# Kernel optimization log

Hardware: AMD Instinct MI355X
Metric: run time of the kernel (lower is better)

## Reference

```python
import jax, jax.numpy as jnp
import numpy as np

B, N, DIM = 32, 1025, 768
H, D = 12, 64
THETA = 100.0


def setup_inputs() -> dict:
    key = jax.random.key(0)
    k0, k1, k2, k3 = jax.random.split(key, 4)
    x = jax.random.normal(k0, (B, N, DIM), dtype=jnp.float32)
    W_qkv = jax.random.normal(k1, (3 * H * D, DIM), dtype=jnp.float32) * 0.02
    W_out = jax.random.normal(k2, (DIM, H * D), dtype=jnp.float32) * 0.02
    b_out = jnp.zeros((DIM,), dtype=jnp.float32)
    # performer random projection buffer: randn(num_features, dim_head) * sqrt(2/dim_head)
    projection = jax.random.normal(k3, (D, D), dtype=jnp.float32) * np.sqrt(2.0 / D)
    # RoPE frequencies for content tokens (n-1 positions, dim_head/2 pairs)
    inv_freq = 1.0 / (THETA ** (np.arange(0, D, 2, dtype=np.float32) / D))  # (D/2,)
    t = np.arange(N - 1, dtype=np.float32)
    angles = np.outer(t, inv_freq)  # (N-1, D/2)
    freqs_cos = jnp.asarray(np.cos(angles), dtype=jnp.float32)
    freqs_sin = jnp.asarray(np.sin(angles), dtype=jnp.float32)
    return {"x": x, "W_qkv": W_qkv, "W_out": W_out, "b_out": b_out,
            "projection": projection, "freqs_cos": freqs_cos, "freqs_sin": freqs_sin}


def reference(x, W_qkv, W_out, b_out, projection, freqs_cos, freqs_sin):
    b, n, _ = x.shape
    h, d = H, D
    # qkv projection and split: 'b n (qkv h d) -> qkv b h n d'
    qkv = jnp.einsum('bnf,gf->bng', x, W_qkv).reshape(b, n, 3, h, d)
    q = jnp.transpose(qkv[:, :, 0], (0, 2, 1, 3))  # (b,h,n,d)
    k = jnp.transpose(qkv[:, :, 1], (0, 2, 1, 3))
    v = jnp.transpose(qkv[:, :, 2], (0, 2, 1, 3))

    def rope(t):
        # rotate content tokens (skip CLS token 0); complex mult as real math
        tc = t[:, :, 1:].reshape(b, h, n - 1, d // 2, 2)
        ev, od = tc[..., 0], tc[..., 1]
        c = freqs_cos[None, None]
        s = freqs_sin[None, None]
        rot = jnp.stack([ev * c - od * s, ev * s + od * c], axis=-1).reshape(b, h, n - 1, d)
        return jnp.concatenate([t[:, :, :1], rot], axis=2)

    q = rope(q)
    k = rope(k)

    def feature_map(t):
        # x * d^{-1/4}, project with (feat, d), relu + eps
        tp = jnp.einsum('bhnd,jd->bhnj', t * (d ** -0.25), projection)
        return jax.nn.relu(tp) + 1e-6

    qf = feature_map(q)
    kf = feature_map(k)

    # non-causal linear attention
    k_sum = kf.sum(axis=-2)                              # (b,h,j)
    context = jnp.einsum('bhnd,bhne->bhde', kf, v)       # (b,h,feat,d)
    D_inv = 1.0 / jnp.einsum('bhnd,bhd->bhn', qf, k_sum)
    out = jnp.einsum('bhde,bhnd,bhn->bhne', context, qf, D_inv)  # (b,h,n,d)

    out = jnp.transpose(out, (0, 2, 1, 3)).reshape(b, n, h * d)
    return jnp.einsum('bnf,gf->bng', out, W_out) + b_out
```

## Files before the change

kernel.cpp:

```cpp
#include <hip/hip_runtime.h>
#include <stdint.h>
#include <stddef.h>

typedef __bf16 bft;
typedef __bf16 bf16x4 __attribute__((ext_vector_type(4)));
typedef __bf16 bf16x8 __attribute__((ext_vector_type(8)));
typedef float f32x4 __attribute__((ext_vector_type(4)));

#define NH 12
#define HD 64
#define SEQ 1025
#define NB 32
#define DMODEL 768
#define MROWS (NB * SEQ)
#define BHN (NB * NH)
#define BSTR 1040
#define MP (NB * BSTR)
#define SEQP 1056

__device__ __forceinline__ void gl_lds16(const void* g, void* l) {
  __builtin_amdgcn_global_load_lds(
      (const __attribute__((address_space(1))) void*)g,
      (__attribute__((address_space(3))) void*)l, 16, 0, 0);
}

__device__ __forceinline__ bf16x4 ds_tr16(const bft* p, int boff) {
  bf16x4 d;
  asm volatile("ds_read_b64_tr_b16 %0, %1 offset:%2"
               : "=v"(d)
               : "v"((const __attribute__((address_space(3))) bft*)p), "i"(boff)
               : "memory");
  return d;
}

__device__ __forceinline__ void lgkm0() {
  asm volatile("s_waitcnt lgkmcnt(0)" ::: "memory");
}

__global__ __launch_bounds__(256) void k_cast(
    const float* __restrict__ S, bft* __restrict__ D, int n4) {
  int i = blockIdx.x * 256 + threadIdx.x;
  if (i < n4) {
    f32x4 v = *(const f32x4*)(S + (size_t)i * 4);
    bf16x4 o;
    o[0] = (bft)v[0]; o[1] = (bft)v[1]; o[2] = (bft)v[2]; o[3] = (bft)v[3];
    *(bf16x4*)(D + (size_t)i * 4) = o;
  }
}

__global__ __launch_bounds__(256) void k_padzero(bft* __restrict__ KFT, bft* __restrict__ VT) {
  int r = blockIdx.x * 256 + threadIdx.x;
  if (r < BHN * 64) {
    bft* a = KFT + (size_t)r * SEQP + 1025;
    bft* b = VT + (size_t)r * SEQP + 1025;
#pragma unroll
    for (int i = 0; i < 31; ++i) { a[i] = (bft)0.f; b[i] = (bft)0.f; }
  }
}

__global__ __launch_bounds__(256) void k_ropeprep(
    const float* __restrict__ FC, const float* __restrict__ FS,
    float* __restrict__ FCP, float* __restrict__ FSP) {
  int i = blockIdx.x * 256 + threadIdx.x;
  if (i < 1040 * 32) {
    int n = i >> 5;
    int fj = i & 31;
    float c = 1.f, s = 0.f;
    if (n >= 1 && n <= 1024) {
      c = FC[(n - 1) * 32 + fj];
      s = FS[(n - 1) * 32 + fj];
    }
    FCP[i] = c;
    FSP[i] = s;
  }
}

__global__ __launch_bounds__(256) void k_qkv_gemm(
    const bft* __restrict__ X, const bft* __restrict__ W,
    const bft* __restrict__ P,
    const float* __restrict__ FCP, const float* __restrict__ FSP,
    bft* __restrict__ QF, bft* __restrict__ KFT, bft* __restrict__ VT) {
  __shared__ __align__(16) bft sA[128 * 64];
  __shared__ __align__(16) bft sB[128 * 64];
  __shared__ __align__(16) bft sP[64 * 64];
  const int tid = threadIdx.x;
  const int lane = tid & 63;
  const int lm = lane & 15;
  const int quad = lane >> 4;
  const int wid = tid >> 6;
  const int wm = (wid & 1) << 6;
  const int wn = (wid >> 1) << 6;
  const int lin = blockIdx.x;
  const int logical = (lin & 7) * 585 + (lin >> 3);
  const int cb = logical % 18;
  const int rb = logical / 18;
  const int m0 = rb * 128;
  const int n0 = cb * 128;
  const int sw = lm & 7;
  const int o0 = (quad ^ sw) << 3;
  const int o1 = ((4 + quad) ^ sw) << 3;

#pragma unroll
  for (int it = 0; it < 2; it++) {
    int c = it * 256 + tid;
    int row = c >> 3;
    int col = ((c & 7) ^ (row & 7)) << 3;
    gl_lds16(P + row * 64 + col, sP + c * 8);
  }

  const bft* aptr[4];
  const bft* bptr[4];
#pragma unroll
  for (int it = 0; it < 4; it++) {
    int c = it * 256 + tid;
    int row = c >> 3;
    int col = ((c & 7) ^ (row & 7)) << 3;
    int ar = m0 + row;
    int b2 = ar / BSTR;
    int nn = ar - b2 * BSTR;
    if (nn > 1024) nn = 1024;
    aptr[it] = X + (size_t)(b2 * SEQ + nn) * DMODEL + col;
    bptr[it] = W + (size_t)(n0 + row) * DMODEL + col;
  }

  f32x4 acc[4][4] = {};

  for (int kt = 0; kt < DMODEL; kt += 64) {
#pragma unroll
    for (int it = 0; it < 4; it++) {
      int c = it * 256 + tid;
      gl_lds16(aptr[it], sA + c * 8);
      gl_lds16(bptr[it], sB + c * 8);
      aptr[it] += 64;
      bptr[it] += 64;
    }
    __syncthreads();
#pragma unroll
    for (int kk = 0; kk < 2; kk++) {
      const int off = kk ? o1 : o0;
      bf16x8 af[4], bb[4];
#pragma unroll
      for (int i = 0; i < 4; i++)
        af[i] = *(const bf16x8*)(sA + (wm + i * 16 + lm) * 64 + off);
#pragma unroll
      for (int j = 0; j < 4; j++)
        bb[j] = *(const bf16x8*)(sB + (wn + j * 16 + lm) * 64 + off);
#pragma unroll
      for (int i = 0; i < 4; i++)
#pragma unroll
        for (int j = 0; j < 4; j++)
          acc[i][j] = __builtin_amdgcn_mfma_f32_16x16x32_bf16(af[i], bb[j], acc[i][j], 0, 0, 0);
    }
    __syncthreads();
  }

  const int s = cb / 6;
  const int h = ((n0 + wn) - s * DMODEL) >> 6;

  bft* tt = sA + wid * 1024;
  const bft* tl = tt + quad * 128 + lm * 4;

  if (s < 2) {
    const float sgn = (lm & 1) ? 1.f : -1.f;
#pragma unroll
    for (int i = 0; i < 4; i++) {
      const int tbase = m0 + wm + i * 16;
      const int bb2 = tbase / BSTR;
      const int nb = tbase - bb2 * BSTR;
#pragma unroll
      for (int j = 0; j < 4; j++) {
        const int fj = (j * 16 + lm) >> 1;
        const int d = j * 16 + lm;
        bf16x4 w;
#pragma unroll
        for (int r = 0; r < 4; r++) {
          float v = acc[i][j][r];
          float pv = __shfl_xor(v, 1);
          int n = nb + quad * 4 + r;
          float cc = FCP[n * 32 + fj];
          float ss = FSP[n * 32 + fj];
          w[r] = (bft)fmaf(pv, sgn * ss, v * cc);
        }
        *(bf16x4*)(tt + d * 16 + quad * 4) = w;
      }
      lgkm0();
      bf16x4 i0a = ds_tr16(tl, 0);
      bf16x4 i0b = ds_tr16(tl, 128);
      bf16x4 i1a = ds_tr16(tl, 1024);
      bf16x4 i1b = ds_tr16(tl, 1152);
      lgkm0();
      __builtin_amdgcn_sched_barrier(0);
      bf16x8 af0, af1;
#pragma unroll
      for (int e = 0; e < 4; e++) {
        af0[e] = i0a[e]; af0[e + 4] = i0b[e];
        af1[e] = i1a[e]; af1[e + 4] = i1b[e];
      }

      if (s == 0) {
        const int n = nb + lm;
        const bool valid = (n < SEQ);
        bft* dst = QF + ((size_t)(bb2 * NH + h) * SEQ + n) * HD;
#pragma unroll
        for (int j2 = 0; j2 < 4; j2++) {
          bf16x8 p0 = *(const bf16x8*)(sP + (j2 * 16 + lm) * 64 + o0);
          bf16x8 p1 = *(const bf16x8*)(sP + (j2 * 16 + lm) * 64 + o1);
          f32x4 fa = {0.f, 0.f, 0.f, 0.f};
          fa = __builtin_amdgcn_mfma_f32_16x16x32_bf16(p0, af0, fa, 0, 0, 0);
          fa = __builtin_amdgcn_mfma_f32_16x16x32_bf16(p1, af1, fa, 0, 0, 0);
          bf16x4 o;
#pragma unroll
          for (int r = 0; r < 4; r++) {
            float v = fa[r] * 0.35355339f;
            o[r] = (bft)(fmaxf(v, 0.f) + 1e-6f);
          }
          if (valid) *(bf16x4*)(dst + j2 * 16 + quad * 4) = o;
        }
      } else {
        const int nq = nb + quad * 4;
#pragma unroll
        for (int j2 = 0; j2 < 4; j2++) {
          bf16x8 p0 = *(const bf16x8*)(sP + (j2 * 16 + lm) * 64 + o0);
          bf16x8 p1 = *(const bf16x8*)(sP + (j2 * 16 + lm) * 64 + o1);
          f32x4 fa = {0.f, 0.f, 0.f, 0.f};
          fa = __builtin_amdgcn_mfma_f32_16x16x32_bf16(af0, p0, fa, 0, 0, 0);
          fa = __builtin_amdgcn_mfma_f32_16x16x32_bf16(af1, p1, fa, 0, 0, 0);
          bf16x4 o;
#pragma unroll
          for (int r = 0; r < 4; r++) {
            float v = fa[r] * 0.35355339f;
            o[r] = (bft)(fmaxf(v, 0.f) + 1e-6f);
          }
          bft* rowp = KFT + ((size_t)(bb2 * NH + h) * 64 + j2 * 16 + lm) * SEQP;
          if (nq + 3 <= 1024) {
            *(bf16x4*)(rowp + nq) = o;
          } else {
#pragma unroll
            for (int r = 0; r < 4; r++)
              if (nq + r <= 1024) rowp[nq + r] = o[r];
          }
        }
      }
    }
  } else {
#pragma unroll
    for (int i = 0; i < 4; i++) {
      const int tbase = m0 + wm + i * 16;
      const int bb2 = tbase / BSTR;
      const int nb = tbase - bb2 * BSTR;
      const int nq = nb + quad * 4;
#pragma unroll
      for (int j = 0; j < 4; j++) {
        bf16x4 o;
#pragma unroll
        for (int r = 0; r < 4; r++) o[r] = (bft)acc[i][j][r];
        bft* rowp = VT + ((size_t)(bb2 * NH + h) * 64 + j * 16 + lm) * SEQP;
        if (nq + 3 <= 1024) {
          *(bf16x4*)(rowp + nq) = o;
        } else {
#pragma unroll
          for (int r = 0; r < 4; r++)
            if (nq + r <= 1024) rowp[nq + r] = o[r];
        }
      }
    }
  }
}

__global__ __launch_bounds__(256) void k_context(
    const bft* __restrict__ KFT, const bft* __restrict__ VT,
    float* __restrict__ CTX, float* __restrict__ KSUM) {
  __shared__ __align__(16) bft sK[64 * 32];
  __shared__ __align__(16) bft sV[64 * 32];
  const int tid = threadIdx.x;
  const int lane = tid & 63;
  const int lm = lane & 15;
  const int quad = lane >> 4;
  const int wid = tid >> 6;
  const int bh = blockIdx.x;
  const int y = blockIdx.y;
  const int c0 = (33 * y) / 4;
  const int c1 = (33 * (y + 1)) / 4;
  const bft* kb = KFT + (size_t)bh * 64 * SEQP;
  const bft* vb = VT + (size_t)bh * 64 * SEQP;
  const int f0 = wid * 16;
  const int srow = tid >> 2;
  const int sch = (tid & 3) * 8;

  bf16x8 ones;
#pragma unroll
  for (int e = 0; e < 8; e++) ones[e] = (bft)1.0f;

  f32x4 acc[4] = {};
  f32x4 ak = {0.f, 0.f, 0.f, 0.f};

  for (int c = c0; c < c1; ++c) {
    const int t0 = c * 32;
    gl_lds16(kb + (size_t)srow * SEQP + t0 + sch, sK + tid * 8);
    gl_lds16(vb + (size_t)srow * SEQP + t0 + sch, sV + tid * 8);
    __syncthreads();
    bf16x8 a = *(const bf16x8*)(sK + (f0 + lm) * 32 + quad * 8);
    ak = __builtin_amdgcn_mfma_f32_16x16x32_bf16(a, ones, ak, 0, 0, 0);
#pragma unroll
    for (int j = 0; j < 4; j++) {
      bf16x8 b = *(const bf16x8*)(sV + (j * 16 + lm) * 32 + quad * 8);
      acc[j] = __builtin_amdgcn_mfma_f32_16x16x32_bf16(a, b, acc[j], 0, 0, 0);
    }
    __syncthreads();
  }

  float* cp = CTX + (size_t)bh * 4096;
#pragma unroll
  for (int j = 0; j < 4; j++)
#pragma unroll
    for (int r = 0; r < 4; r++)
      atomicAdd(&cp[(f0 + quad * 4 + r) * 64 + j * 16 + lm], acc[j][r]);
  if (lm == 0) {
#pragma unroll
    for (int r = 0; r < 4; r++)
      atomicAdd(&KSUM[bh * 64 + f0 + quad * 4 + r], ak[r]);
  }
}

__global__ __launch_bounds__(256) void k_ctxprep(
    const float* __restrict__ CTX, const float* __restrict__ KSUM,
    bft* __restrict__ CTH, bft* __restrict__ CTL,
    bft* __restrict__ KTH, bft* __restrict__ KTL) {
  const int bh = blockIdx.x;
  const int tid = threadIdx.x;
  const int e = tid >> 2;
  const int g = tid & 3;
  const float* src = CTX + (size_t)bh * 4096 + e;
  bf16x8 h0, l0, h1, l1;
#pragma unroll
  for (int k = 0; k < 16; ++k) {
    float v = src[(g * 16 + k) * 64];
    bft hi = (bft)v;
    bft lo = (bft)(v - (float)hi);
    if (k < 8) { h0[k] = hi; l0[k] = lo; }
    else       { h1[k - 8] = hi; l1[k - 8] = lo; }
  }
  const int c0 = (2 * g) ^ (e & 7);
  const int c1 = (2 * g + 1) ^ (e & 7);
  bft* dh = CTH + (size_t)bh * 4096 + e * 64;
  bft* dl = CTL + (size_t)bh * 4096 + e * 64;
  *(bf16x8*)(dh + c0 * 8) = h0;
  *(bf16x8*)(dh + c1 * 8) = h1;
  *(bf16x8*)(dl + c0 * 8) = l0;
  *(bf16x8*)(dl + c1 * 8) = l1;
  if (tid < 64) {
    float v = KSUM[bh * 64 + tid];
    bft hi = (bft)v;
    KTH[bh * 64 + tid] = hi;
    KTL[bh * 64 + tid] = (bft)(v - (float)hi);
  }
}

__global__ __launch_bounds__(256) void k_qside(
    const bft* __restrict__ QF, const bft* __restrict__ CTH,
    const bft* __restrict__ CTL, const bft* __restrict__ KTH,
    const bft* __restrict__ KTL, bft* __restrict__ ATTN) {
  __shared__ __align__(16) bft sq[128 * 64];
  __shared__ __align__(16) bft sh[64 * 64];
  __shared__ __align__(16) bft sl[64 * 64];
  const int tid = threadIdx.x;
  const int lane = tid & 63;
  const int lm = lane & 15;
  const int quad = lane >> 4;
  const int wid = tid >> 6;
  const int bh = blockIdx.x;
  const int n0 = blockIdx.y * 128;
  const bft* qf = QF + ((size_t)bh * SEQ + n0) * HD;

#pragma unroll
  for (int it = 0; it < 4; it++) {
    int c = it * 256 + tid;
    int row = c >> 3;
    int col = ((c & 7) ^ (row & 7)) << 3;
    gl_lds16(qf + (size_t)row * 64 + col, sq + c * 8);
  }
#pragma unroll
  for (int it = 0; it < 2; it++) {
    int c = it * 256 + tid;
    gl_lds16(CTH + (size_t)bh * 4096 + c * 8, sh + c * 8);
    gl_lds16(CTL + (size_t)bh * 4096 + c * 8, sl + c * 8);
  }
  bf16x8 kh0 = *(const bf16x8*)(KTH + bh * 64 + quad * 8);
  bf16x8 kh1 = *(const bf16x8*)(KTH + bh * 64 + 32 + quad * 8);
  bf16x8 kl0 = *(const bf16x8*)(KTL + bh * 64 + quad * 8);
  bf16x8 kl1 = *(const bf16x8*)(KTL + bh * 64 + 32 + quad * 8);
  bf16x8 zz = {};
  bf16x8 ad0 = (lm == 0) ? kh0 : (lm == 1) ? kl0 : zz;
  bf16x8 ad1 = (lm == 0) ? kh1 : (lm == 1) ? kl1 : zz;
  __syncthreads();

  bf16x8 ah[4][2], al[4][2];
#pragma unroll
  for (int eb = 0; eb < 4; eb++)
#pragma unroll
    for (int kc = 0; kc < 2; kc++) {
      const int off = ((quad + 4 * kc) ^ (lm & 7)) * 8;
      ah[eb][kc] = *(const bf16x8*)(sh + (eb * 16 + lm) * 64 + off);
      al[eb][kc] = *(const bf16x8*)(sl + (eb * 16 + lm) * 64 + off);
    }

  const int b = bh / NH;
  const int h = bh - b * NH;
#pragma unroll
  for (int tb2 = 0; tb2 < 2; tb2++) {
    const int tok0 = (wid * 2 + tb2) * 16;
    const int roff = (tok0 + lm) * 64;
    bf16x8 bq0 = *(const bf16x8*)(sq + roff + ((quad) ^ (lm & 7)) * 8);
    bf16x8 bq1 = *(const bf16x8*)(sq + roff + ((4 + quad) ^ (lm & 7)) * 8);
    f32x4 dacc = {0.f, 0.f, 0.f, 0.f};
    dacc = __builtin_amdgcn_mfma_f32_16x16x32_bf16(ad0, bq0, dacc, 0, 0, 0);
    dacc = __builtin_amdgcn_mfma_f32_16x16x32_bf16(ad1, bq1, dacc, 0, 0, 0);
    const float den = __shfl(dacc[0] + dacc[1], lm);
    const float dinv = 1.0f / den;
    f32x4 fa[4] = {};
#pragma unroll
    for (int eb = 0; eb < 4; eb++) {
      fa[eb] = __builtin_amdgcn_mfma_f32_16x16x32_bf16(ah[eb][0], bq0, fa[eb], 0, 0, 0);
      fa[eb] = __builtin_amdgcn_mfma_f32_16x16x32_bf16(al[eb][0], bq0, fa[eb], 0, 0, 0);
      fa[eb] = __builtin_amdgcn_mfma_f32_16x16x32_bf16(ah[eb][1], bq1, fa[eb], 0, 0, 0);
      fa[eb] = __builtin_amdgcn_mfma_f32_16x16x32_bf16(al[eb][1], bq1, fa[eb], 0, 0, 0);
    }
    const int n = n0 + tok0 + lm;
    if (n < SEQ) {
      bft* dst = ATTN + ((size_t)(b * SEQ + n)) * DMODEL + h * 64;
#pragma unroll
      for (int eb = 0; eb < 4; eb++) {
        bf16x4 o;
#pragma unroll
        for (int r = 0; r < 4; r++) o[r] = (bft)(fa[eb][r] * dinv);
        *(bf16x4*)(dst + eb * 16 + quad * 4) = o;
      }
    }
  }
}

__global__ __launch_bounds__(256) void k_out_gemm(
    const bft* __restrict__ A, const bft* __restrict__ W,
    const float* __restrict__ BIAS, float* __restrict__ OUT) {
  __shared__ __align__(16) bft sA[128 * 64];
  __shared__ __align__(16) bft sB[128 * 64];
  const int tid = threadIdx.x;
  const int lane = tid & 63;
  const int lm = lane & 15;
  const int quad = lane >> 4;
  const int wid = tid >> 6;
  const int wm = (wid & 1) << 6;
  const int wn = (wid >> 1) << 6;
  const int lin = blockIdx.x;
  const int xcd = lin & 7;
  const int slot = lin >> 3;
  const int base = (xcd < 6) ? xcd * 193 : 6 * 193 + (xcd - 6) * 192;
  const int logical = base + slot;
  const int cb = logical % 6;
  const int rb = logical / 6;
  const int m0 = rb * 128;
  const int n0 = cb * 128;
  const int sw = lm & 7;
  const int o0 = (quad ^ sw) << 3;
  const int o1 = ((4 + quad) ^ sw) << 3;

  const bft* aptr[4];
  const bft* bptr[4];
#pragma unroll
  for (int it = 0; it < 4; it++) {
    int c = it * 256 + tid;
    int row = c >> 3;
    int col = ((c & 7) ^ (row & 7)) << 3;
    int ar = m0 + row;
    if (ar >= MROWS) ar = MROWS - 1;
    aptr[it] = A + (size_t)ar * DMODEL + col;
    bptr[it] = W + (size_t)(n0 + row) * DMODEL + col;
  }

  f32x4 acc[4][4] = {};

  for (int kt = 0; kt < DMODEL; kt += 64) {
#pragma unroll
    for (int it = 0; it < 4; it++) {
      int c = it * 256 + tid;
      gl_lds16(aptr[it], sA + c * 8);
      gl_lds16(bptr[it], sB + c * 8);
      aptr[it] += 64;
      bptr[it] += 64;
    }
    __syncthreads();
#pragma unroll
    for (int kk = 0; kk < 2; kk++) {
      const int off = kk ? o1 : o0;
      bf16x8 af[4], bb[4];
#pragma unroll
      for (int i = 0; i < 4; i++)
        af[i] = *(const bf16x8*)(sA + (wm + i * 16 + lm) * 64 + off);
#pragma unroll
      for (int j = 0; j < 4; j++)
        bb[j] = *(const bf16x8*)(sB + (wn + j * 16 + lm) * 64 + off);
#pragma unroll
      for (int i = 0; i < 4; i++)
#pragma unroll
        for (int j = 0; j < 4; j++)
          acc[i][j] = __builtin_amdgcn_mfma_f32_16x16x32_bf16(bb[j], af[i], acc[i][j], 0, 0, 0);
    }
    __syncthreads();
  }

#pragma unroll
  for (int i = 0; i < 4; i++) {
    const int m = m0 + wm + i * 16 + lm;
    if (m < MROWS) {
#pragma unroll
      for (int j = 0; j < 4; j++) {
        const int g = n0 + wn + j * 16 + quad * 4;
        f32x4 bias = *(const f32x4*)(BIAS + g);
        f32x4 o;
#pragma unroll
        for (int r = 0; r < 4; r++) o[r] = acc[i][j][r] + bias[r];
        *(f32x4*)(OUT + (size_t)m * DMODEL + g) = o;
      }
    }
  }
}

extern "C" void kernel_launch(void* const* d_in, const int* in_sizes, int n_in,
                              void* d_out, int out_size, void* d_ws, size_t ws_size,
                              hipStream_t stream) {
  const float* x = (const float*)d_in[0];
  const float* wqkv = (const float*)d_in[1];
  const float* wout = (const float*)d_in[2];
  const float* bout = (const float*)d_in[3];
  const float* proj = (const float*)d_in[4];
  const float* fc = (const float*)d_in[5];
  const float* fs = (const float*)d_in[6];
  float* outp = (float*)d_out;

  char* ws = (char*)d_ws;
  const size_t xb_bytes = (size_t)MROWS * DMODEL * 2;
  const size_t qf_bytes = (size_t)BHN * SEQ * HD * 2;
  const size_t kt_bytes = (size_t)BHN * 64 * SEQP * 2;
  const size_t wqkvb_bytes = (size_t)3 * DMODEL * DMODEL * 2;
  const size_t woutb_bytes = (size_t)DMODEL * DMODEL * 2;
  const size_t projb_bytes = 8192;
  const size_t ctx_bytes = (size_t)BHN * 64 * 64 * 4;
  const size_t ks_bytes = (size_t)BHN * 64 * 4;
  const size_t ctt_bytes = (size_t)BHN * 64 * 64 * 2;
  const size_t kst_bytes = (size_t)BHN * 64 * 2;
  const size_t ftab_bytes = (size_t)1040 * 32 * 4;

  bft* xb = (bft*)ws;
  bft* qfb = (bft*)(ws + xb_bytes);
  bft* kft = (bft*)(ws + xb_bytes + qf_bytes);
  bft* vt = (bft*)(ws + xb_bytes + qf_bytes + kt_bytes);
  bft* wqkvb = (bft*)(ws + xb_bytes + qf_bytes + 2 * kt_bytes);
  bft* woutb = (bft*)(ws + xb_bytes + qf_bytes + 2 * kt_bytes + wqkvb_bytes);
  bft* projb = (bft*)(ws + xb_bytes + qf_bytes + 2 * kt_bytes + wqkvb_bytes + woutb_bytes);
  float* fcp = (float*)(ws + xb_bytes + qf_bytes + 2 * kt_bytes + wqkvb_bytes + woutb_bytes + projb_bytes);
  float* fsp = (float*)(ws + xb_bytes + qf_bytes + 2 * kt_bytes + wqkvb_bytes + woutb_bytes + projb_bytes + ftab_bytes);

  float* ctx = (float*)ws;
  float* ksum = (float*)(ws + ctx_bytes);
  bft* cth = (bft*)(ws + ctx_bytes + ks_bytes);
  bft* ctl = (bft*)(ws + ctx_bytes + ks_bytes + ctt_bytes);
  bft* kth = (bft*)(ws + ctx_bytes + ks_bytes + 2 * ctt_bytes);
  bft* ktl = (bft*)(ws + ctx_bytes + ks_bytes + 2 * ctt_bytes + kst_bytes);
  bft* attn = kft;

  dim3 blk(256);
  k_cast<<<dim3((MROWS * DMODEL / 4 + 255) / 256), blk, 0, stream>>>(x, xb, MROWS * DMODEL / 4);
  k_cast<<<dim3((3 * DMODEL * DMODEL / 4 + 255) / 256), blk, 0, stream>>>(wqkv, wqkvb, 3 * DMODEL * DMODEL / 4);
  k_cast<<<dim3((DMODEL * DMODEL / 4 + 255) / 256), blk, 0, stream>>>(wout, woutb, DMODEL * DMODEL / 4);
  k_cast<<<dim3((HD * HD / 4 + 255) / 256), blk, 0, stream>>>(proj, projb, HD * HD / 4);
  k_padzero<<<dim3((BHN * 64 + 255) / 256), blk, 0, stream>>>(kft, vt);
  k_ropeprep<<<dim3(130), blk, 0, stream>>>(fc, fs, fcp, fsp);

  k_qkv_gemm<<<dim3(4680), blk, 0, stream>>>(xb, wqkvb, projb, fcp, fsp, qfb, kft, vt);

  hipMemsetAsync(ctx, 0, ctx_bytes + ks_bytes, stream);

  k_context<<<dim3(BHN, 4), blk, 0, stream>>>(kft, vt, ctx, ksum);
  k_ctxprep<<<dim3(BHN), blk, 0, stream>>>(ctx, ksum, cth, ctl, kth, ktl);
  k_qside<<<dim3(BHN, 9), blk, 0, stream>>>(qfb, cth, ctl, kth, ktl, attn);
  k_out_gemm<<<dim3(1542), blk, 0, stream>>>(attn, woutb, bout, outp);
  (void)in_sizes; (void)n_in; (void)out_size; (void)ws_size;
}
```

Baseline: 515.9 us.

## Fuse prep kernels, drop atomics and LDS staging in context and q-side kernels

```diff
diff --git a/kernel.cpp b/kernel.cpp
--- a/kernel.cpp
+++ b/kernel.cpp
@@ -37,41 +37,57 @@
   asm volatile("s_waitcnt lgkmcnt(0)" ::: "memory");
 }
 
-__global__ __launch_bounds__(256) void k_cast(
-    const float* __restrict__ S, bft* __restrict__ D, int n4) {
-  int i = blockIdx.x * 256 + threadIdx.x;
-  if (i < n4) {
-    f32x4 v = *(const f32x4*)(S + (size_t)i * 4);
-    bf16x4 o;
-    o[0] = (bft)v[0]; o[1] = (bft)v[1]; o[2] = (bft)v[2]; o[3] = (bft)v[3];
-    *(bf16x4*)(D + (size_t)i * 4) = o;
-  }
-}
-
-__global__ __launch_bounds__(256) void k_padzero(bft* __restrict__ KFT, bft* __restrict__ VT) {
-  int r = blockIdx.x * 256 + threadIdx.x;
-  if (r < BHN * 64) {
+#define S0P 6297600
+#define S1P (S0P + 442368)
+#define S2P (S1P + 147456)
+#define S3P (S2P + 1024)
+#define S4P (S3P + 24576)
+#define S5P (S4P + 33280)
+
+__global__ __launch_bounds__(256) void k_prep(
+    const float* __restrict__ X, const float* __restrict__ WQKV,
+    const float* __restrict__ WOUT, const float* __restrict__ PROJ,
+    const float* __restrict__ FC, const float* __restrict__ FS,
+    bft* __restrict__ XB, bft* __restrict__ WQKVB, bft* __restrict__ WOUTB,
+    bft* __restrict__ PROJB, bft* __restrict__ KFT, bft* __restrict__ VT,
+    float* __restrict__ FCP, float* __restrict__ FSP) {
+  const int i = blockIdx.x * 256 + threadIdx.x;
+  if (i < S0P) {
+    f32x4 v = *(const f32x4*)(X + (size_t)i * 4);
+    bf16x4 o; o[0]=(bft)v[0]; o[1]=(bft)v[1]; o[2]=(bft)v[2]; o[3]=(bft)v[3];
+    *(bf16x4*)(XB + (size_t)i * 4) = o;
+  } else if (i < S1P) {
+    int k = i - S0P;
+    f32x4 v = *(const f32x4*)(WQKV + (size_t)k * 4);
+    bf16x4 o; o[0]=(bft)v[0]; o[1]=(bft)v[1]; o[2]=(bft)v[2]; o[3]=(bft)v[3];
+    *(bf16x4*)(WQKVB + (size_t)k * 4) = o;
+  } else if (i < S2P) {
+    int k = i - S1P;
+    f32x4 v = *(const f32x4*)(WOUT + (size_t)k * 4);
+    bf16x4 o; o[0]=(bft)v[0]; o[1]=(bft)v[1]; o[2]=(bft)v[2]; o[3]=(bft)v[3];
+    *(bf16x4*)(WOUTB + (size_t)k * 4) = o;
+  } else if (i < S3P) {
+    int k = i - S2P;
+    f32x4 v = *(const f32x4*)(PROJ + (size_t)k * 4);
+    bf16x4 o; o[0]=(bft)v[0]; o[1]=(bft)v[1]; o[2]=(bft)v[2]; o[3]=(bft)v[3];
+    *(bf16x4*)(PROJB + (size_t)k * 4) = o;
+  } else if (i < S4P) {
+    int r = i - S3P;
     bft* a = KFT + (size_t)r * SEQP + 1025;
     bft* b = VT + (size_t)r * SEQP + 1025;
 #pragma unroll
-    for (int i = 0; i < 31; ++i) { a[i] = (bft)0.f; b[i] = (bft)0.f; }
-  }
-}
-
-__global__ __launch_bounds__(256) void k_ropeprep(
-    const float* __restrict__ FC, const float* __restrict__ FS,
-    float* __restrict__ FCP, float* __restrict__ FSP) {
-  int i = blockIdx.x * 256 + threadIdx.x;
-  if (i < 1040 * 32) {
-    int n = i >> 5;
-    int fj = i & 31;
+    for (int q = 0; q < 31; ++q) { a[q] = (bft)0.f; b[q] = (bft)0.f; }
+  } else if (i < S5P) {
+    int k = i - S4P;
+    int n = k >> 5;
+    int fj = k & 31;
     float c = 1.f, s = 0.f;
     if (n >= 1 && n <= 1024) {
       c = FC[(n - 1) * 32 + fj];
       s = FS[(n - 1) * 32 + fj];
     }
-    FCP[i] = c;
-    FSP[i] = s;
+    FCP[k] = c;
+    FSP[k] = s;
   }
 }
 
@@ -80,9 +96,9 @@
     const bft* __restrict__ P,
     const float* __restrict__ FCP, const float* __restrict__ FSP,
     bft* __restrict__ QF, bft* __restrict__ KFT, bft* __restrict__ VT) {
-  __shared__ __align__(16) bft sA[128 * 64];
-  __shared__ __align__(16) bft sB[128 * 64];
-  __shared__ __align__(16) bft sP[64 * 64];
+  __shared__ __align__(16) bft sAll[128 * 64 * 2];
+  bft* sA = sAll;
+  bft* sB = sAll + 8192;
   const int tid = threadIdx.x;
   const int lane = tid & 63;
   const int lm = lane & 15;
@@ -100,14 +116,6 @@
   const int o0 = (quad ^ sw) << 3;
   const int o1 = ((4 + quad) ^ sw) << 3;
 
-#pragma unroll
-  for (int it = 0; it < 2; it++) {
-    int c = it * 256 + tid;
-    int row = c >> 3;
-    int col = ((c & 7) ^ (row & 7)) << 3;
-    gl_lds16(P + row * 64 + col, sP + c * 8);
-  }
-
   const bft* aptr[4];
   const bft* bptr[4];
 #pragma unroll
@@ -157,81 +165,94 @@
   const int s = cb / 6;
   const int h = ((n0 + wn) - s * DMODEL) >> 6;
 
-  bft* tt = sA + wid * 1024;
+  bft* tt = sAll + wid * 4096;
   const bft* tl = tt + quad * 128 + lm * 4;
 
   if (s < 2) {
     const float sgn = (lm & 1) ? 1.f : -1.f;
+    int bb2s[4], nbs[4];
 #pragma unroll
     for (int i = 0; i < 4; i++) {
       const int tbase = m0 + wm + i * 16;
-      const int bb2 = tbase / BSTR;
-      const int nb = tbase - bb2 * BSTR;
+      bb2s[i] = tbase / BSTR;
+      nbs[i] = tbase - bb2s[i] * BSTR;
 #pragma unroll
       for (int j = 0; j < 4; j++) {
-        const int fj = (j * 16 + lm) >> 1;
         const int d = j * 16 + lm;
+        const int fj = d >> 1;
         bf16x4 w;
 #pragma unroll
         for (int r = 0; r < 4; r++) {
           float v = acc[i][j][r];
           float pv = __shfl_xor(v, 1);
-          int n = nb + quad * 4 + r;
+          int n = nbs[i] + quad * 4 + r;
           float cc = FCP[n * 32 + fj];
           float ss = FSP[n * 32 + fj];
           w[r] = (bft)fmaf(pv, sgn * ss, v * cc);
         }
-        *(bf16x4*)(tt + d * 16 + quad * 4) = w;
-      }
-      lgkm0();
-      bf16x4 i0a = ds_tr16(tl, 0);
-      bf16x4 i0b = ds_tr16(tl, 128);
-      bf16x4 i1a = ds_tr16(tl, 1024);
-      bf16x4 i1b = ds_tr16(tl, 1152);
-      lgkm0();
-      __builtin_amdgcn_sched_barrier(0);
-      bf16x8 af0, af1;
+        *(bf16x4*)(tt + i * 1024 + d * 16 + quad * 4) = w;
+      }
+    }
+    lgkm0();
+    bf16x4 t0[4], t1[4], t2[4], t3[4];
+#pragma unroll
+    for (int i = 0; i < 4; i++) {
+      t0[i] = ds_tr16(tl, i * 2048 + 0);
+      t1[i] = ds_tr16(tl, i * 2048 + 128);
+      t2[i] = ds_tr16(tl, i * 2048 + 1024);
+      t3[i] = ds_tr16(tl, i * 2048 + 1152);
+    }
+    lgkm0();
+    __builtin_amdgcn_sched_barrier(0);
+    bf16x8 af[4][2];
+#pragma unroll
+    for (int i = 0; i < 4; i++) {
 #pragma unroll
       for (int e = 0; e < 4; e++) {
-        af0[e] = i0a[e]; af0[e + 4] = i0b[e];
-        af1[e] = i1a[e]; af1[e + 4] = i1b[e];
-      }
-
-      if (s == 0) {
-        const int n = nb + lm;
-        const bool valid = (n < SEQ);
-        bft* dst = QF + ((size_t)(bb2 * NH + h) * SEQ + n) * HD;
-#pragma unroll
-        for (int j2 = 0; j2 < 4; j2++) {
-          bf16x8 p0 = *(const bf16x8*)(sP + (j2 * 16 + lm) * 64 + o0);
-          bf16x8 p1 = *(const bf16x8*)(sP + (j2 * 16 + lm) * 64 + o1);
+        af[i][0][e] = t0[i][e]; af[i][0][e + 4] = t1[i][e];
+        af[i][1][e] = t2[i][e]; af[i][1][e + 4] = t3[i][e];
+      }
+    }
+
+    if (s == 0) {
+#pragma unroll
+      for (int j2 = 0; j2 < 4; j2++) {
+        bf16x8 p0 = *(const bf16x8*)(P + (j2 * 16 + lm) * 64 + quad * 8);
+        bf16x8 p1 = *(const bf16x8*)(P + (j2 * 16 + lm) * 64 + 32 + quad * 8);
+#pragma unroll
+        for (int i = 0; i < 4; i++) {
           f32x4 fa = {0.f, 0.f, 0.f, 0.f};
-          fa = __builtin_amdgcn_mfma_f32_16x16x32_bf16(p0, af0, fa, 0, 0, 0);
-          fa = __builtin_amdgcn_mfma_f32_16x16x32_bf16(p1, af1, fa, 0, 0, 0);
+          fa = __builtin_amdgcn_mfma_f32_16x16x32_bf16(p0, af[i][0], fa, 0, 0, 0);
+          fa = __builtin_amdgcn_mfma_f32_16x16x32_bf16(p1, af[i][1], fa, 0, 0, 0);
           bf16x4 o;
 #pragma unroll
           for (int r = 0; r < 4; r++) {
             float v = fa[r] * 0.35355339f;
             o[r] = (bft)(fmaxf(v, 0.f) + 1e-6f);
           }
-          if (valid) *(bf16x4*)(dst + j2 * 16 + quad * 4) = o;
+          const int n = nbs[i] + lm;
+          if (n < SEQ)
+            *(bf16x4*)(QF + ((size_t)(bb2s[i] * NH + h) * SEQ + n) * HD + j2 * 16 + quad * 4) = o;
         }
-      } else {
-        const int nq = nb + quad * 4;
-#pragma unroll
-        for (int j2 = 0; j2 < 4; j2++) {
-          bf16x8 p0 = *(const bf16x8*)(sP + (j2 * 16 + lm) * 64 + o0);
-          bf16x8 p1 = *(const bf16x8*)(sP + (j2 * 16 + lm) * 64 + o1);
+      }
+    } else {
+#pragma unroll
+      for (int j2 = 0; j2 < 4; j2++) {
+        bf16x8 p0 = *(const bf16x8*)(P + (j2 * 16 + lm) * 64 + quad * 8);
+        bf16x8 p1 = *(const bf16x8*)(P + (j2 * 16 + lm) * 64 + 32 + quad * 8);
+#pragma unroll
+        for (int i = 0; i < 4; i++) {
           f32x4 fa = {0.f, 0.f, 0.f, 0.f};
-          fa = __builtin_amdgcn_mfma_f32_16x16x32_bf16(af0, p0, fa, 0, 0, 0);
-          fa = __builtin_amdgcn_mfma_f32_16x16x32_bf16(af1, p1, fa, 0, 0, 0);
+          fa = __builtin_amdgcn_mfma_f32_16x16x32_bf16(af[i][0], p0, fa, 0, 0, 0);
+          fa = __builtin_amdgcn_mfma_f32_16x16x32_bf16(af[i][1], p1, fa, 0, 0, 0);
           bf16x4 o;
 #pragma unroll
           for (int r = 0; r < 4; r++) {
             float v = fa[r] * 0.35355339f;
             o[r] = (bft)(fmaxf(v, 0.f) + 1e-6f);
           }
-          bft* rowp = KFT + ((size_t)(bb2 * NH + h) * 64 + j2 * 16 + lm) * SEQP;
+          const int nq = nbs[i] + quad * 4;
+          bft* rowp = KFT + ((size_t)(bb2s[i] * NH + h) * 64 + j2 * 16 + lm) * SEQP;
           if (nq + 3 <= 1024) {
             *(bf16x4*)(rowp + nq) = o;
           } else {
@@ -269,9 +290,7 @@
 
 __global__ __launch_bounds__(256) void k_context(
     const bft* __restrict__ KFT, const bft* __restrict__ VT,
-    float* __restrict__ CTX, float* __restrict__ KSUM) {
-  __shared__ __align__(16) bft sK[64 * 32];
-  __shared__ __align__(16) bft sV[64 * 32];
+    float* __restrict__ CTXP, float* __restrict__ KSP) {
   const int tid = threadIdx.x;
   const int lane = tid & 63;
   const int lm = lane & 15;
@@ -281,11 +300,9 @@
   const int y = blockIdx.y;
   const int c0 = (33 * y) / 4;
   const int c1 = (33 * (y + 1)) / 4;
-  const bft* kb = KFT + (size_t)bh * 64 * SEQP;
-  const bft* vb = VT + (size_t)bh * 64 * SEQP;
+  const bft* kb = KFT + (size_t)bh * 64 * SEQP + (size_t)(wid * 16 + lm) * SEQP + quad * 8;
+  const bft* vb = VT + (size_t)bh * 64 * SEQP + (size_t)lm * SEQP + quad * 8;
   const int f0 = wid * 16;
-  const int srow = tid >> 2;
-  const int sch = (tid & 3) * 8;
 
   bf16x8 ones;
 #pragma unroll
@@ -294,62 +311,64 @@
   f32x4 acc[4] = {};
   f32x4 ak = {0.f, 0.f, 0.f, 0.f};
 
+#pragma unroll 2
   for (int c = c0; c < c1; ++c) {
     const int t0 = c * 32;
-    gl_lds16(kb + (size_t)srow * SEQP + t0 + sch, sK + tid * 8);
-    gl_lds16(vb + (size_t)srow * SEQP + t0 + sch, sV + tid * 8);
-    __syncthreads();
-    bf16x8 a = *(const bf16x8*)(sK + (f0 + lm) * 32 + quad * 8);
+    bf16x8 a = *(const bf16x8*)(kb + t0);
     ak = __builtin_amdgcn_mfma_f32_16x16x32_bf16(a, ones, ak, 0, 0, 0);
 #pragma unroll
     for (int j = 0; j < 4; j++) {
-      bf16x8 b = *(const bf16x8*)(sV + (j * 16 + lm) * 32 + quad * 8);
+      bf16x8 b = *(const bf16x8*)(vb + (size_t)j * 16 * SEQP + t0);
       acc[j] = __builtin_amdgcn_mfma_f32_16x16x32_bf16(a, b, acc[j], 0, 0, 0);
     }
-    __syncthreads();
-  }
-
-  float* cp = CTX + (size_t)bh * 4096;
+  }
+
+  float* cp = CTXP + ((size_t)(y * BHN) + bh) * 4096;
 #pragma unroll
   for (int j = 0; j < 4; j++)
-#pragma unroll
-    for (int r = 0; r < 4; r++)
-      atomicAdd(&cp[(f0 + quad * 4 + r) * 64 + j * 16 + lm], acc[j][r]);
-  if (lm == 0) {
-#pragma unroll
-    for (int r = 0; r < 4; r++)
-      atomicAdd(&KSUM[bh * 64 + f0 + quad * 4 + r], ak[r]);
-  }
+    *(f32x4*)(cp + (j * 16 + lm) * 64 + f0 + quad * 4) = acc[j];
+  if (lm == 0)
+    *(f32x4*)(KSP + ((size_t)(y * BHN) + bh) * 64 + f0 + quad * 4) = ak;
 }
 
 __global__ __launch_bounds__(256) void k_ctxprep(
-    const float* __restrict__ CTX, const float* __restrict__ KSUM,
+    const float* __restrict__ CTXP, const float* __restrict__ KSP,
     bft* __restrict__ CTH, bft* __restrict__ CTL,
     bft* __restrict__ KTH, bft* __restrict__ KTL) {
   const int bh = blockIdx.x;
   const int tid = threadIdx.x;
   const int e = tid >> 2;
-  const int g = tid & 3;
-  const float* src = CTX + (size_t)bh * 4096 + e;
+  const int fc = tid & 3;
+  f32x4 s[4] = {};
+#pragma unroll
+  for (int y = 0; y < 4; y++) {
+    const float* src = CTXP + ((size_t)(y * BHN) + bh) * 4096 + e * 64 + fc * 16;
+#pragma unroll
+    for (int q = 0; q < 4; q++) {
+      f32x4 v = *(const f32x4*)(src + q * 4);
+      s[q][0] += v[0]; s[q][1] += v[1]; s[q][2] += v[2]; s[q][3] += v[3];
+    }
+  }
   bf16x8 h0, l0, h1, l1;
 #pragma unroll
-  for (int k = 0; k < 16; ++k) {
-    float v = src[(g * 16 + k) * 64];
+  for (int k = 0; k < 8; k++) {
+    float v = s[k >> 2][k & 3];
     bft hi = (bft)v;
-    bft lo = (bft)(v - (float)hi);
-    if (k < 8) { h0[k] = hi; l0[k] = lo; }
-    else       { h1[k - 8] = hi; l1[k - 8] = lo; }
-  }
-  const int c0 = (2 * g) ^ (e & 7);
-  const int c1 = (2 * g + 1) ^ (e & 7);
-  bft* dh = CTH + (size_t)bh * 4096 + e * 64;
-  bft* dl = CTL + (size_t)bh * 4096 + e * 64;
-  *(bf16x8*)(dh + c0 * 8) = h0;
-  *(bf16x8*)(dh + c1 * 8) = h1;
-  *(bf16x8*)(dl + c0 * 8) = l0;
-  *(bf16x8*)(dl + c1 * 8) = l1;
+    h0[k] = hi; l0[k] = (bft)(v - (float)hi);
+    float v2 = s[2 + (k >> 2)][k & 3];
+    bft hi2 = (bft)v2;
+    h1[k] = hi2; l1[k] = (bft)(v2 - (float)hi2);
+  }
+  bft* dh = CTH + (size_t)bh * 4096 + e * 64 + fc * 16;
+  bft* dl = CTL + (size_t)bh * 4096 + e * 64 + fc * 16;
+  *(bf16x8*)(dh) = h0;
+  *(bf16x8*)(dh + 8) = h1;
+  *(bf16x8*)(dl) = l0;
+  *(bf16x8*)(dl + 8) = l1;
   if (tid < 64) {
-    float v = KSUM[bh * 64 + tid];
+    float v = 0.f;
+#pragma unroll
+    for (int y = 0; y < 4; y++) v += KSP[((size_t)(y * BHN) + bh) * 64 + tid];
     bft hi = (bft)v;
     KTH[bh * 64 + tid] = hi;
     KTL[bh * 64 + tid] = (bft)(v - (float)hi);
@@ -360,9 +379,6 @@
     const bft* __restrict__ QF, const bft* __restrict__ CTH,
     const bft* __restrict__ CTL, const bft* __restrict__ KTH,
     const bft* __restrict__ KTL, bft* __restrict__ ATTN) {
-  __shared__ __align__(16) bft sq[128 * 64];
-  __shared__ __align__(16) bft sh[64 * 64];
-  __shared__ __align__(16) bft sl[64 * 64];
   const int tid = threadIdx.x;
   const int lane = tid & 63;
   const int lm = lane & 15;
@@ -372,19 +388,6 @@
   const int n0 = blockIdx.y * 128;
   const bft* qf = QF + ((size_t)bh * SEQ + n0) * HD;
 
-#pragma unroll
-  for (int it = 0; it < 4; it++) {
-    int c = it * 256 + tid;
-    int row = c >> 3;
-    int col = ((c & 7) ^ (row & 7)) << 3;
-    gl_lds16(qf + (size_t)row * 64 + col, sq + c * 8);
-  }
-#pragma unroll
-  for (int it = 0; it < 2; it++) {
-    int c = it * 256 + tid;
-    gl_lds16(CTH + (size_t)bh * 4096 + c * 8, sh + c * 8);
-    gl_lds16(CTL + (size_t)bh * 4096 + c * 8, sl + c * 8);
-  }
   bf16x8 kh0 = *(const bf16x8*)(KTH + bh * 64 + quad * 8);
   bf16x8 kh1 = *(const bf16x8*)(KTH + bh * 64 + 32 + quad * 8);
   bf16x8 kl0 = *(const bf16x8*)(KTL + bh * 64 + quad * 8);
@@ -392,16 +395,15 @@
   bf16x8 zz = {};
   bf16x8 ad0 = (lm == 0) ? kh0 : (lm == 1) ? kl0 : zz;
   bf16x8 ad1 = (lm == 0) ? kh1 : (lm == 1) ? kl1 : zz;
-  __syncthreads();
 
   bf16x8 ah[4][2], al[4][2];
 #pragma unroll
   for (int eb = 0; eb < 4; eb++)
 #pragma unroll
     for (int kc = 0; kc < 2; kc++) {
-      const int off = ((quad + 4 * kc) ^ (lm & 7)) * 8;
-      ah[eb][kc] = *(const bf16x8*)(sh + (eb * 16 + lm) * 64 + off);
-      al[eb][kc] = *(const bf16x8*)(sl + (eb * 16 + lm) * 64 + off);
+      const size_t off = (size_t)bh * 4096 + (eb * 16 + lm) * 64 + kc * 32 + quad * 8;
+      ah[eb][kc] = *(const bf16x8*)(CTH + off);
+      al[eb][kc] = *(const bf16x8*)(CTL + off);
     }
 
   const int b = bh / NH;
@@ -409,9 +411,9 @@
 #pragma unroll
   for (int tb2 = 0; tb2 < 2; tb2++) {
     const int tok0 = (wid * 2 + tb2) * 16;
-    const int roff = (tok0 + lm) * 64;
-    bf16x8 bq0 = *(const bf16x8*)(sq + roff + ((quad) ^ (lm & 7)) * 8);
-    bf16x8 bq1 = *(const bf16x8*)(sq + roff + ((4 + quad) ^ (lm & 7)) * 8);
+    const int rr = (n0 + tok0 + lm <= 1024) ? (tok0 + lm) : (1024 - n0);
+    bf16x8 bq0 = *(const bf16x8*)(qf + (size_t)rr * 64 + quad * 8);
+    bf16x8 bq1 = *(const bf16x8*)(qf + (size_t)rr * 64 + 32 + quad * 8);
     f32x4 dacc = {0.f, 0.f, 0.f, 0.f};
     dacc = __builtin_amdgcn_mfma_f32_16x16x32_bf16(ad0, bq0, dacc, 0, 0, 0);
     dacc = __builtin_amdgcn_mfma_f32_16x16x32_bf16(ad1, bq1, dacc, 0, 0, 0);
@@ -544,8 +546,8 @@
   const size_t wqkvb_bytes = (size_t)3 * DMODEL * DMODEL * 2;
   const size_t woutb_bytes = (size_t)DMODEL * DMODEL * 2;
   const size_t projb_bytes = 8192;
-  const size_t ctx_bytes = (size_t)BHN * 64 * 64 * 4;
-  const size_t ks_bytes = (size_t)BHN * 64 * 4;
+  const size_t ctxp_bytes = (size_t)4 * BHN * 4096 * 4;
+  const size_t ksp_bytes = (size_t)4 * BHN * 64 * 4;
   const size_t ctt_bytes = (size_t)BHN * 64 * 64 * 2;
   const size_t kst_bytes = (size_t)BHN * 64 * 2;
   const size_t ftab_bytes = (size_t)1040 * 32 * 4;
@@ -560,28 +562,20 @@
   float* fcp = (float*)(ws + xb_bytes + qf_bytes + 2 * kt_bytes + wqkvb_bytes + woutb_bytes + projb_bytes);
   float* fsp = (float*)(ws + xb_bytes + qf_bytes + 2 * kt_bytes + wqkvb_bytes + woutb_bytes + projb_bytes + ftab_bytes);
 
-  float* ctx = (float*)ws;
-  float* ksum = (float*)(ws + ctx_bytes);
-  bft* cth = (bft*)(ws + ctx_bytes + ks_bytes);
-  bft* ctl = (bft*)(ws + ctx_bytes + ks_bytes + ctt_bytes);
-  bft* kth = (bft*)(ws + ctx_bytes + ks_bytes + 2 * ctt_bytes);
-  bft* ktl = (bft*)(ws + ctx_bytes + ks_bytes + 2 * ctt_bytes + kst_bytes);
+  float* ctxp = (float*)ws;
+  float* ksp = (float*)(ws + ctxp_bytes);
+  bft* cth = (bft*)(ws + ctxp_bytes + ksp_bytes);
+  bft* ctl = (bft*)(ws + ctxp_bytes + ksp_bytes + ctt_bytes);
+  bft* kth = (bft*)(ws + ctxp_bytes + ksp_bytes + 2 * ctt_bytes);
+  bft* ktl = (bft*)(ws + ctxp_bytes + ksp_bytes + 2 * ctt_bytes + kst_bytes);
   bft* attn = kft;
 
   dim3 blk(256);
-  k_cast<<<dim3((MROWS * DMODEL / 4 + 255) / 256), blk, 0, stream>>>(x, xb, MROWS * DMODEL / 4);
-  k_cast<<<dim3((3 * DMODEL * DMODEL / 4 + 255) / 256), blk, 0, stream>>>(wqkv, wqkvb, 3 * DMODEL * DMODEL / 4);
-  k_cast<<<dim3((DMODEL * DMODEL / 4 + 255) / 256), blk, 0, stream>>>(wout, woutb, DMODEL * DMODEL / 4);
-  k_cast<<<dim3((HD * HD / 4 + 255) / 256), blk, 0, stream>>>(proj, projb, HD * HD / 4);
-  k_padzero<<<dim3((BHN * 64 + 255) / 256), blk, 0, stream>>>(kft, vt);
-  k_ropeprep<<<dim3(130), blk, 0, stream>>>(fc, fs, fcp, fsp);
-
+  k_prep<<<dim3((S5P + 255) / 256), blk, 0, stream>>>(
+      x, wqkv, wout, proj, fc, fs, xb, wqkvb, woutb, projb, kft, vt, fcp, fsp);
   k_qkv_gemm<<<dim3(4680), blk, 0, stream>>>(xb, wqkvb, projb, fcp, fsp, qfb, kft, vt);
-
-  hipMemsetAsync(ctx, 0, ctx_bytes + ks_bytes, stream);
-
-  k_context<<<dim3(BHN, 4), blk, 0, stream>>>(kft, vt, ctx, ksum);
-  k_ctxprep<<<dim3(BHN), blk, 0, stream>>>(ctx, ksum, cth, ctl, kth, ktl);
+  k_context<<<dim3(BHN, 4), blk, 0, stream>>>(kft, vt, ctxp, ksp);
+  k_ctxprep<<<dim3(BHN), blk, 0, stream>>>(ctxp, ksp, cth, ctl, kth, ktl);
   k_qside<<<dim3(BHN, 9), blk, 0, stream>>>(qfb, cth, ctl, kth, ktl, attn);
   k_out_gemm<<<dim3(1542), blk, 0, stream>>>(attn, woutb, bout, outp);
   (void)in_sizes; (void)n_in; (void)out_size; (void)ws_size;
```

Result: no change. 518.0 us (+0.4%).
